# Kernel optimization log

Measured on AMD Instinct MI355X. Metric: run time of the kernel, lower is better.

Reference implementation:

```python
import jax, jax.numpy as jnp
import numpy as np

B, L, FT, FS, H = 32, 4096, 512, 512, 512  # batch, seq, text feat, summary feat, hidden
C = FT + FS + 1  # conv1 in-channels (num_features + 1 coverage channel)


def setup_inputs() -> dict:
    key = jax.random.key(0)
    ks = jax.random.split(key, 8)
    text_states = jax.random.normal(ks[0], (B, L, FT), dtype=jnp.float32)
    summary_current_state = jax.random.normal(ks[1], (B, FS), dtype=jnp.float32)
    coverage = jax.random.uniform(ks[2], (B, 1, L), dtype=jnp.float32)
    W1 = jax.random.normal(ks[3], (H, C), dtype=jnp.float32) * (1.0 / np.sqrt(C))
    b1 = jnp.zeros((H,), dtype=jnp.float32)
    W2 = jax.random.normal(ks[4], (1, H), dtype=jnp.float32) * (1.0 / np.sqrt(H))
    b2 = jnp.zeros((1,), dtype=jnp.float32)
    text_length = jax.random.randint(ks[5], (B,), 1, L + 1)  # >=1 so softmax is defined
    return {
        "text_states": text_states,
        "summary_current_state": summary_current_state,
        "coverage": coverage,
        "W1": W1,
        "b1": b1,
        "W2": W2,
        "b2": b2,
        "text_length": text_length,
    }


def reference(text_states, summary_current_state, coverage, W1, b1, W2, b2, text_length):
    b, l, ft = text_states.shape
    ts = jnp.swapaxes(text_states, -1, -2)  # [B, FT, L]
    ss = jnp.broadcast_to(summary_current_state[..., None],
                          summary_current_state.shape + (l,))  # [B, FS, L]
    x = jnp.concatenate([ts, ss, coverage], axis=-2)  # [B, C, L]
    # kernel-size-1 Conv1d == pointwise linear over channels
    h = jnp.tanh(jnp.einsum('bcl,hc->bhl', x, W1) + b1[None, :, None])  # [B, H, L]
    logits = jnp.einsum('bhl,oh->bol', h, W2) + b2[None, :, None]  # [B, 1, L]
    mask = jnp.arange(l)[None, None, :] < text_length[:, None, None]  # [B, 1, L]
    masked = jnp.where(mask, logits, -jnp.inf)
    attention = jax.nn.softmax(masked, axis=-1)  # [B, 1, L]
    context_vector = jnp.sum(attention * ts, axis=-1)  # [B, FT]
    return context_vector, attention
```

## Files before the change

### kernel.cpp

```cpp
#include <hip/hip_runtime.h>
#include <cstdint>
#include <cstddef>

#define B_  32
#define L_  4096
#define FT_ 512
#define FS_ 512
#define H_  512
#define C_  1025

typedef __attribute__((ext_vector_type(8))) short short8;
typedef __attribute__((ext_vector_type(4))) float float4v;

__device__ __forceinline__ short f2bf(float f) {
    union { float f; unsigned u; } v; v.f = f;
    unsigned r = v.u + 0x7FFF + ((v.u >> 16) & 1);
    return (short)(r >> 16);
}

__device__ __forceinline__ float fast_tanh(float x) {
    float e = __expf(2.f * x);
    return 1.f - 2.f * __builtin_amdgcn_rcpf(e + 1.f);
}

__global__ __launch_bounds__(256) void prep_kernel(
        const float* __restrict__ W1, const float* __restrict__ summary,
        const float* __restrict__ b1, short* __restrict__ fragB,
        float* __restrict__ w1c, float* __restrict__ sconst) {
    if (blockIdx.x < 128) {
        int gid = blockIdx.x * 256 + threadIdx.x;
        int lane = gid & 63;
        int ts_  = gid >> 6;
        int t = ts_ >> 4;
        int s = ts_ & 15;
        int h  = t * 16 + (lane & 15);
        int k0 = s * 32 + (lane >> 4) * 8;
        const float* src = W1 + (size_t)h * C_ + k0;
        short8 o;
        #pragma unroll
        for (int j = 0; j < 8; ++j) o[j] = f2bf(src[j]);
        *(short8*)(fragB + (size_t)gid * 8) = o;
        if (gid < H_) w1c[gid] = W1[(size_t)gid * C_ + FT_ + FS_];
    } else {
        int wid  = ((blockIdx.x - 128) * 256 + threadIdx.x) >> 6;
        int lane = threadIdx.x & 63;
        int b = wid >> 9;
        int h = wid & 511;
        const float* wrow = W1 + (size_t)h * C_ + FT_;
        const float* srow = summary + (size_t)b * FS_;
        float acc = 0.f;
        #pragma unroll
        for (int f = lane; f < FS_; f += 64) acc += wrow[f] * srow[f];
        #pragma unroll
        for (int off = 32; off > 0; off >>= 1) acc += __shfl_down(acc, off, 64);
        if (lane == 0) sconst[wid] = acc + b1[h];
    }
}

#define TL 64
__global__ __launch_bounds__(512, 4) void logits_kernel(
        const float* __restrict__ ts, const float* __restrict__ coverage,
        const int* __restrict__ text_length,
        const short* __restrict__ fragB, const float* __restrict__ w1c,
        const float* __restrict__ sconst, const float* __restrict__ W2,
        const float* __restrict__ b2, float* __restrict__ logits) {
    const int b  = blockIdx.y;
    const int l0 = blockIdx.x * TL;
    const int len = text_length[b];
    if (l0 >= len) return;

    __shared__ short ts_lds[TL * 512];

    const float4* src = (const float4*)(ts + ((size_t)b * L_ + l0) * FT_);
    for (int j = threadIdx.x; j < TL * 64; j += 512) {
        int l = j >> 6;
        int g = j & 63;
        float4 v0 = src[2 * j];
        float4 v1 = src[2 * j + 1];
        short8 p;
        p[0] = f2bf(v0.x); p[1] = f2bf(v0.y); p[2] = f2bf(v0.z); p[3] = f2bf(v0.w);
        p[4] = f2bf(v1.x); p[5] = f2bf(v1.y); p[6] = f2bf(v1.z); p[7] = f2bf(v1.w);
        *(short8*)(ts_lds + l * 512 + ((g ^ (l & 7)) << 3)) = p;
    }
    __syncthreads();

    const int lane = threadIdx.x & 63;
    const int wv   = threadIdx.x >> 6;
    const int col  = lane & 15;
    const int quad = lane >> 4;
    const int swz  = col & 7;

    const short* aBase = ts_lds + col * 512;
    const short* bBase = fragB + (size_t)(wv * 64) * 512 + lane * 8;

    float4v acc[4][4];
    #pragma unroll
    for (int nt = 0; nt < 4; ++nt)
        #pragma unroll
        for (int mt = 0; mt < 4; ++mt)
            acc[nt][mt] = (float4v){0.f, 0.f, 0.f, 0.f};

    #pragma unroll 2
    for (int ks = 0; ks < 16; ++ks) {
        short8 af[4];
        const int ag = ((ks * 4 + quad) ^ swz) << 3;
        #pragma unroll
        for (int mt = 0; mt < 4; ++mt)
            af[mt] = *(const short8*)(aBase + mt * (16 * 512) + ag);
        short8 bf[4];
        #pragma unroll
        for (int nt = 0; nt < 4; ++nt)
            bf[nt] = *(const short8*)(bBase + (size_t)(nt * 16 + ks) * 512);
        #pragma unroll
        for (int nt = 0; nt < 4; ++nt)
            #pragma unroll
            for (int mt = 0; mt < 4; ++mt)
                acc[nt][mt] = __builtin_amdgcn_mfma_f32_16x16x32_bf16(
                    af[mt], bf[nt], acc[nt][mt], 0, 0, 0);
    }

    const int h0 = wv * 64;
    const float* sc_b = sconst + (size_t)b * H_;
    float4 cov[4];
    #pragma unroll
    for (int mt = 0; mt < 4; ++mt)
        cov[mt] = *(const float4*)(coverage + (size_t)b * L_ + l0 + mt * 16 + quad * 4);

    float partial[4][4];
    #pragma unroll
    for (int mt = 0; mt < 4; ++mt)
        #pragma unroll
        for (int r = 0; r < 4; ++r) partial[mt][r] = 0.f;

    #pragma unroll
    for (int nt = 0; nt < 4; ++nt) {
        const int h = h0 + nt * 16 + col;
        const float sc = sc_b[h];
        const float wc = w1c[h];
        const float w2 = W2[h];
        #pragma unroll
        for (int mt = 0; mt < 4; ++mt)
            #pragma unroll
            for (int r = 0; r < 4; ++r) {
                float pre = acc[nt][mt][r] + sc + wc * ((const float*)&cov[mt])[r];
                partial[mt][r] += w2 * fast_tanh(pre);
            }
    }

    #pragma unroll
    for (int mt = 0; mt < 4; ++mt)
        #pragma unroll
        for (int r = 0; r < 4; ++r) {
            float v = partial[mt][r];
            v += __shfl_xor(v, 8, 64);
            v += __shfl_xor(v, 4, 64);
            v += __shfl_xor(v, 2, 64);
            v += __shfl_xor(v, 1, 64);
            partial[mt][r] = v;
        }

    __syncthreads();
    float* red = (float*)ts_lds;
    if (col == 0) {
        #pragma unroll
        for (int mt = 0; mt < 4; ++mt)
            #pragma unroll
            for (int r = 0; r < 4; ++r)
                red[wv * 64 + mt * 16 + quad * 4 + r] = partial[mt][r];
    }
    __syncthreads();
    if (threadIdx.x < 64) {
        const int lg = l0 + threadIdx.x;
        if (lg < len) {
            float s = b2[0];
            #pragma unroll
            for (int w = 0; w < 8; ++w) s += red[w * 64 + threadIdx.x];
            logits[(size_t)b * L_ + lg] = s;
        }
    }
}

__global__ __launch_bounds__(1024) void softmax_kernel(
        const float* __restrict__ logits, const int* __restrict__ text_length,
        float* __restrict__ attn_out) {
    const int b = blockIdx.x;
    const int len = text_length[b];
    const float* lg = logits + (size_t)b * L_;
    float* at = attn_out + (size_t)b * L_;
    __shared__ float sred[1024];

    float m = -INFINITY;
    for (int l = threadIdx.x; l < len; l += 1024) m = fmaxf(m, lg[l]);
    sred[threadIdx.x] = m;
    __syncthreads();
    for (int s = 512; s > 0; s >>= 1) {
        if (threadIdx.x < s)
            sred[threadIdx.x] = fmaxf(sred[threadIdx.x], sred[threadIdx.x + s]);
        __syncthreads();
    }
    m = sred[0];
    __syncthreads();

    float sum = 0.f;
    for (int l = threadIdx.x; l < len; l += 1024) sum += __expf(lg[l] - m);
    sred[threadIdx.x] = sum;
    __syncthreads();
    for (int s = 512; s > 0; s >>= 1) {
        if (threadIdx.x < s) sred[threadIdx.x] += sred[threadIdx.x + s];
        __syncthreads();
    }
    const float inv = 1.f / sred[0];

    for (int l = threadIdx.x; l < L_; l += 1024)
        at[l] = (l < len) ? __expf(lg[l] - m) * inv : 0.f;
}

#define LC 256
__global__ __launch_bounds__(256) void context_partial_kernel(
        const float* __restrict__ ts, const float* __restrict__ attn,
        const int* __restrict__ text_length, float* __restrict__ cpart) {
    const int b = blockIdx.y;
    const int c = blockIdx.x;
    const int l0 = c * LC;
    const int len = text_length[b];
    const int lpar = threadIdx.x >> 7;
    const int f4   = threadIdx.x & 127;
    float4 acc = {0.f, 0.f, 0.f, 0.f};
    if (l0 < len) {
        const int lend = min(len, l0 + LC);
        const float* at = attn + (size_t)b * L_;
        const float4* row = (const float4*)(ts + ((size_t)b * L_ + l0 + lpar) * FT_) + f4;
        for (int l = l0 + lpar; l < lend; l += 2, row += 256) {
            const float a = at[l];
            float4 v = *row;
            acc.x += a * v.x; acc.y += a * v.y;
            acc.z += a * v.z; acc.w += a * v.w;
        }
    }
    ((float4*)cpart)[(size_t)(((b * 16 + c) * 2 + lpar)) * 128 + f4] = acc;
}

__global__ __launch_bounds__(128) void context_reduce_kernel(
        const float* __restrict__ cpart, float* __restrict__ ctx) {
    const int b = blockIdx.x;
    const int t = threadIdx.x;
    float4 s = {0.f, 0.f, 0.f, 0.f};
    const float4* p = (const float4*)cpart + (size_t)b * 32 * 128 + t;
    #pragma unroll
    for (int c = 0; c < 32; ++c) {
        float4 v = p[c * 128];
        s.x += v.x; s.y += v.y; s.z += v.z; s.w += v.w;
    }
    ((float4*)ctx)[(size_t)b * 128 + t] = s;
}

extern "C" void kernel_launch(void* const* d_in, const int* in_sizes, int n_in,
                              void* d_out, int out_size, void* d_ws, size_t ws_size,
                              hipStream_t stream) {
    const float* ts       = (const float*)d_in[0];
    const float* summary  = (const float*)d_in[1];
    const float* coverage = (const float*)d_in[2];
    const float* W1       = (const float*)d_in[3];
    const float* b1       = (const float*)d_in[4];
    const float* W2       = (const float*)d_in[5];
    const float* b2       = (const float*)d_in[6];
    const int*   text_len = (const int*)d_in[7];

    float* ctx_out  = (float*)d_out;
    float* attn_out = (float*)d_out + B_ * FT_;

    char* ws = (char*)d_ws;
    short* fragB  = (short*)(ws);
    float* w1c    = (float*)(ws + 524288);
    float* sconst = (float*)(ws + 526336);
    float* logits = (float*)(ws + 591872);
    float* cpart  = (float*)(ws + 1116160);

    prep_kernel<<<128 + 4096, 256, 0, stream>>>(W1, summary, b1, fragB, w1c, sconst);
    logits_kernel<<<dim3(L_ / TL, B_), 512, 0, stream>>>(
        ts, coverage, text_len, fragB, w1c, sconst, W2, b2, logits);
    softmax_kernel<<<B_, 1024, 0, stream>>>(logits, text_len, attn_out);
    context_partial_kernel<<<dim3(L_ / LC, B_), 256, 0, stream>>>(
        ts, attn_out, text_len, cpart);
    context_reduce_kernel<<<B_, 128, 0, stream>>>(cpart, ctx_out);
}
```

Baseline: 425.2 us.

## Shrink logits tile to 32 rows with 4 waves; fuse softmax normalize into context pass

The logits kernel tile drops from 64 to 32 sequence rows with 256 threads. Each of the 4 waves now covers 128 hidden units (8x2 MFMA tiles) instead of 64. This halves LDS use per block and doubles the number of blocks, which should raise occupancy and spread work better across masked-off sequence tails, at the cost of reading more W1 fragments per output row. The softmax kernel now writes only per-batch max and inverse sum, and the context kernel (chunk size halved to 128) computes the attention values itself, writes them out, and uses them from shared memory. This removes one full read and write pass over the attention array.

```diff
diff --git a/kernel.cpp b/kernel.cpp
--- a/kernel.cpp
+++ b/kernel.cpp
@@ -57,8 +57,8 @@
     }
 }
 
-#define TL 64
-__global__ __launch_bounds__(512, 4) void logits_kernel(
+#define TL 32
+__global__ __launch_bounds__(256, 4) void logits_kernel(
         const float* __restrict__ ts, const float* __restrict__ coverage,
         const int* __restrict__ text_length,
         const short* __restrict__ fragB, const float* __restrict__ w1c,
@@ -72,7 +72,7 @@
     __shared__ short ts_lds[TL * 512];
 
     const float4* src = (const float4*)(ts + ((size_t)b * L_ + l0) * FT_);
-    for (int j = threadIdx.x; j < TL * 64; j += 512) {
+    for (int j = threadIdx.x; j < TL * 64; j += 256) {
         int l = j >> 6;
         int g = j & 63;
         float4 v0 = src[2 * j];
@@ -91,55 +91,53 @@
     const int swz  = col & 7;
 
     const short* aBase = ts_lds + col * 512;
-    const short* bBase = fragB + (size_t)(wv * 64) * 512 + lane * 8;
-
-    float4v acc[4][4];
-    #pragma unroll
-    for (int nt = 0; nt < 4; ++nt)
-        #pragma unroll
-        for (int mt = 0; mt < 4; ++mt)
+    const short* bBase = fragB + (size_t)(wv * 8) * 16 * 512 + lane * 8;
+
+    float4v acc[8][2];
+    #pragma unroll
+    for (int nt = 0; nt < 8; ++nt)
+        #pragma unroll
+        for (int mt = 0; mt < 2; ++mt)
             acc[nt][mt] = (float4v){0.f, 0.f, 0.f, 0.f};
 
     #pragma unroll 2
     for (int ks = 0; ks < 16; ++ks) {
-        short8 af[4];
+        short8 af[2];
         const int ag = ((ks * 4 + quad) ^ swz) << 3;
         #pragma unroll
-        for (int mt = 0; mt < 4; ++mt)
+        for (int mt = 0; mt < 2; ++mt)
             af[mt] = *(const short8*)(aBase + mt * (16 * 512) + ag);
-        short8 bf[4];
-        #pragma unroll
-        for (int nt = 0; nt < 4; ++nt)
-            bf[nt] = *(const short8*)(bBase + (size_t)(nt * 16 + ks) * 512);
-        #pragma unroll
-        for (int nt = 0; nt < 4; ++nt)
-            #pragma unroll
-            for (int mt = 0; mt < 4; ++mt)
+        #pragma unroll
+        for (int nt = 0; nt < 8; ++nt) {
+            short8 bf = *(const short8*)(bBase + (size_t)(nt * 16 + ks) * 512);
+            #pragma unroll
+            for (int mt = 0; mt < 2; ++mt)
                 acc[nt][mt] = __builtin_amdgcn_mfma_f32_16x16x32_bf16(
-                    af[mt], bf[nt], acc[nt][mt], 0, 0, 0);
-    }
-
-    const int h0 = wv * 64;
+                    af[mt], bf, acc[nt][mt], 0, 0, 0);
+        }
+    }
+
+    const int h0 = wv * 128;
     const float* sc_b = sconst + (size_t)b * H_;
-    float4 cov[4];
-    #pragma unroll
-    for (int mt = 0; mt < 4; ++mt)
+    float4 cov[2];
+    #pragma unroll
+    for (int mt = 0; mt < 2; ++mt)
         cov[mt] = *(const float4*)(coverage + (size_t)b * L_ + l0 + mt * 16 + quad * 4);
 
-    float partial[4][4];
-    #pragma unroll
-    for (int mt = 0; mt < 4; ++mt)
+    float partial[2][4];
+    #pragma unroll
+    for (int mt = 0; mt < 2; ++mt)
         #pragma unroll
         for (int r = 0; r < 4; ++r) partial[mt][r] = 0.f;
 
     #pragma unroll
-    for (int nt = 0; nt < 4; ++nt) {
+    for (int nt = 0; nt < 8; ++nt) {
         const int h = h0 + nt * 16 + col;
         const float sc = sc_b[h];
         const float wc = w1c[h];
         const float w2 = W2[h];
         #pragma unroll
-        for (int mt = 0; mt < 4; ++mt)
+        for (int mt = 0; mt < 2; ++mt)
             #pragma unroll
             for (int r = 0; r < 4; ++r) {
                 float pre = acc[nt][mt][r] + sc + wc * ((const float*)&cov[mt])[r];
@@ -148,7 +146,7 @@
     }
 
     #pragma unroll
-    for (int mt = 0; mt < 4; ++mt)
+    for (int mt = 0; mt < 2; ++mt)
         #pragma unroll
         for (int r = 0; r < 4; ++r) {
             float v = partial[mt][r];
@@ -163,30 +161,29 @@
     float* red = (float*)ts_lds;
     if (col == 0) {
         #pragma unroll
-        for (int mt = 0; mt < 4; ++mt)
+        for (int mt = 0; mt < 2; ++mt)
             #pragma unroll
             for (int r = 0; r < 4; ++r)
-                red[wv * 64 + mt * 16 + quad * 4 + r] = partial[mt][r];
-    }
-    __syncthreads();
-    if (threadIdx.x < 64) {
+                red[wv * 32 + mt * 16 + quad * 4 + r] = partial[mt][r];
+    }
+    __syncthreads();
+    if (threadIdx.x < 32) {
         const int lg = l0 + threadIdx.x;
         if (lg < len) {
             float s = b2[0];
             #pragma unroll
-            for (int w = 0; w < 8; ++w) s += red[w * 64 + threadIdx.x];
+            for (int w = 0; w < 4; ++w) s += red[w * 32 + threadIdx.x];
             logits[(size_t)b * L_ + lg] = s;
         }
     }
 }
 
-__global__ __launch_bounds__(1024) void softmax_kernel(
+__global__ __launch_bounds__(1024) void softmax_stats_kernel(
         const float* __restrict__ logits, const int* __restrict__ text_length,
-        float* __restrict__ attn_out) {
+        float2* __restrict__ stats) {
     const int b = blockIdx.x;
     const int len = text_length[b];
     const float* lg = logits + (size_t)b * L_;
-    float* at = attn_out + (size_t)b * L_;
     __shared__ float sred[1024];
 
     float m = -INFINITY;
@@ -209,35 +206,47 @@
         if (threadIdx.x < s) sred[threadIdx.x] += sred[threadIdx.x + s];
         __syncthreads();
     }
-    const float inv = 1.f / sred[0];
-
-    for (int l = threadIdx.x; l < L_; l += 1024)
-        at[l] = (l < len) ? __expf(lg[l] - m) * inv : 0.f;
-}
-
-#define LC 256
-__global__ __launch_bounds__(256) void context_partial_kernel(
-        const float* __restrict__ ts, const float* __restrict__ attn,
-        const int* __restrict__ text_length, float* __restrict__ cpart) {
+    if (threadIdx.x == 0) {
+        float2 st; st.x = m; st.y = 1.f / sred[0];
+        stats[b] = st;
+    }
+}
+
+#define LC 128
+__global__ __launch_bounds__(256) void context_kernel(
+        const float* __restrict__ ts, const float* __restrict__ logits,
+        const float2* __restrict__ stats, const int* __restrict__ text_length,
+        float* __restrict__ attn_out, float* __restrict__ cpart) {
     const int b = blockIdx.y;
     const int c = blockIdx.x;
     const int l0 = c * LC;
     const int len = text_length[b];
+    const float2 st = stats[b];
+
+    __shared__ float a_s[LC];
+    if (threadIdx.x < LC) {
+        const int l = l0 + threadIdx.x;
+        float a = 0.f;
+        if (l < len) a = __expf(logits[(size_t)b * L_ + l] - st.x) * st.y;
+        a_s[threadIdx.x] = a;
+        attn_out[(size_t)b * L_ + l] = a;
+    }
+    __syncthreads();
+
     const int lpar = threadIdx.x >> 7;
     const int f4   = threadIdx.x & 127;
     float4 acc = {0.f, 0.f, 0.f, 0.f};
     if (l0 < len) {
-        const int lend = min(len, l0 + LC);
-        const float* at = attn + (size_t)b * L_;
+        const int lend = min(len - l0, LC);
         const float4* row = (const float4*)(ts + ((size_t)b * L_ + l0 + lpar) * FT_) + f4;
-        for (int l = l0 + lpar; l < lend; l += 2, row += 256) {
-            const float a = at[l];
+        for (int i = lpar; i < lend; i += 2, row += 256) {
+            const float a = a_s[i];
             float4 v = *row;
             acc.x += a * v.x; acc.y += a * v.y;
             acc.z += a * v.z; acc.w += a * v.w;
         }
     }
-    ((float4*)cpart)[(size_t)(((b * 16 + c) * 2 + lpar)) * 128 + f4] = acc;
+    ((float4*)cpart)[(size_t)((b * 32 + c) * 2 + lpar) * 128 + f4] = acc;
 }
 
 __global__ __launch_bounds__(128) void context_reduce_kernel(
@@ -245,9 +254,9 @@
     const int b = blockIdx.x;
     const int t = threadIdx.x;
     float4 s = {0.f, 0.f, 0.f, 0.f};
-    const float4* p = (const float4*)cpart + (size_t)b * 32 * 128 + t;
-    #pragma unroll
-    for (int c = 0; c < 32; ++c) {
+    const float4* p = (const float4*)cpart + (size_t)b * 64 * 128 + t;
+    #pragma unroll
+    for (int c = 0; c < 64; ++c) {
         float4 v = p[c * 128];
         s.x += v.x; s.y += v.y; s.z += v.z; s.w += v.w;
     }
@@ -270,17 +279,18 @@
     float* attn_out = (float*)d_out + B_ * FT_;
 
     char* ws = (char*)d_ws;
-    short* fragB  = (short*)(ws);
-    float* w1c    = (float*)(ws + 524288);
-    float* sconst = (float*)(ws + 526336);
-    float* logits = (float*)(ws + 591872);
-    float* cpart  = (float*)(ws + 1116160);
+    short*  fragB  = (short*)(ws);
+    float*  w1c    = (float*)(ws + 524288);
+    float*  sconst = (float*)(ws + 526336);
+    float*  logits = (float*)(ws + 591872);
+    float2* stats  = (float2*)(ws + 1116160);
+    float*  cpart  = (float*)(ws + 1116672);
 
     prep_kernel<<<128 + 4096, 256, 0, stream>>>(W1, summary, b1, fragB, w1c, sconst);
-    logits_kernel<<<dim3(L_ / TL, B_), 512, 0, stream>>>(
+    logits_kernel<<<dim3(L_ / TL, B_), 256, 0, stream>>>(
         ts, coverage, text_len, fragB, w1c, sconst, W2, b2, logits);
-    softmax_kernel<<<B_, 1024, 0, stream>>>(logits, text_len, attn_out);
-    context_partial_kernel<<<dim3(L_ / LC, B_), 256, 0, stream>>>(
-        ts, attn_out, text_len, cpart);
+    softmax_stats_kernel<<<B_, 1024, 0, stream>>>(logits, text_len, stats);
+    context_kernel<<<dim3(L_ / LC, B_), 256, 0, stream>>>(
+        ts, logits, stats, text_len, attn_out, cpart);
     context_reduce_kernel<<<B_, 128, 0, stream>>>(cpart, ctx_out);
 }
```

Result: no change. 420.2 us (-1.2%).
